# Kernel optimization log

Hardware: AMD Instinct MI355X
Metric: run time of the kernel (lower is better)

Reference implementation:

```python
import jax, jax.numpy as jnp
import numpy as np

EMBED = 768
HEADS = 12
HEAD_DIM = EMBED // HEADS
SCALE = HEAD_DIM ** -0.5


def setup_inputs() -> dict:
    key = jax.random.key(0)
    k1, k2, k3, k4, k5 = jax.random.split(key, 5)
    x = jax.random.normal(k1, (4, 2048, EMBED), dtype=jnp.float32)
    w_qkv = jax.random.normal(k2, (EMBED, 3 * EMBED), dtype=jnp.float32) * (EMBED ** -0.5)
    b_qkv = jax.random.normal(k3, (3 * EMBED,), dtype=jnp.float32) * 0.02
    w_proj = jax.random.normal(k4, (EMBED, EMBED), dtype=jnp.float32) * (EMBED ** -0.5)
    b_proj = jax.random.normal(k5, (EMBED,), dtype=jnp.float32) * 0.02
    return {"x": x, "w_qkv": w_qkv, "b_qkv": b_qkv, "w_proj": w_proj, "b_proj": b_proj}


def reference(x, w_qkv, b_qkv, w_proj, b_proj):
    B, T, D = x.shape
    qkv = x @ w_qkv + b_qkv                      # [B, T, 3D]
    qkv = qkv.reshape(B, T, 3, HEADS, HEAD_DIM)
    qkv = jnp.transpose(qkv, (2, 0, 3, 1, 4))    # [3, B, H, T, hd]
    q, k, v = qkv[0], qkv[1], qkv[2]
    scores = jnp.einsum('bhqd,bhkd->bhqk', q, k) * SCALE
    attn = jax.nn.softmax(scores, axis=-1)       # dropout p=0.0 -> identity
    out = jnp.einsum('bhqk,bhkd->bhqd', attn, v)
    out = jnp.transpose(out, (0, 2, 1, 3)).reshape(B, T, D)
    return out @ w_proj + b_proj
```

## Files before the change

kernel.cpp:

```cpp
#include <hip/hip_runtime.h>
#include <hip/hip_bf16.h>

#define EMBED 768
#define HEADS 12
#define HD 64
#define BATCH 4
#define SEQ 2048
#define M_TOK (BATCH*SEQ)
#define N_QKV (3*EMBED)
#define SL2E 0.18033688011112042f

typedef short bf8 __attribute__((ext_vector_type(8)));
typedef float f4  __attribute__((ext_vector_type(4)));
typedef unsigned short us8 __attribute__((ext_vector_type(8)));

static __device__ inline unsigned short f2bf(float f) {
    unsigned int x = __float_as_uint(f);
    unsigned int r = (x + 0x7fffu + ((x >> 16) & 1u)) >> 16;
    return (unsigned short)r;
}

static __device__ inline unsigned int pack2bf(float a, float b) {
#if defined(__has_builtin)
#if __has_builtin(__builtin_amdgcn_cvt_pk_bf16_f32)
    auto r = __builtin_amdgcn_cvt_pk_bf16_f32(a, b);
    return __builtin_bit_cast(unsigned int, r);
#else
    unsigned int ua = (__float_as_uint(a) + 0x8000u) >> 16;
    unsigned int ub = (__float_as_uint(b) + 0x8000u) & 0xffff0000u;
    return ua | ub;
#endif
#else
    unsigned int ua = (__float_as_uint(a) + 0x8000u) >> 16;
    unsigned int ub = (__float_as_uint(b) + 0x8000u) & 0xffff0000u;
    return ua | ub;
#endif
}

#define GLD_LDS(gp, lp) __builtin_amdgcn_global_load_lds( \
    (const __attribute__((address_space(1))) void*)(gp),  \
    (__attribute__((address_space(3))) void*)(lp), 16, 0, 0)

__global__ void cvt_f32_bf16(const float* __restrict__ in,
                             unsigned short* __restrict__ out, int n) {
    int i = (blockIdx.x * blockDim.x + threadIdx.x) * 4;
    if (i < n) {
        float4 v = *reinterpret_cast<const float4*>(in + i);
        ushort4 o;
        o.x = f2bf(v.x); o.y = f2bf(v.y); o.z = f2bf(v.z); o.w = f2bf(v.w);
        *reinterpret_cast<ushort4*>(out + i) = o;
    }
}

__global__ void transpose_f32_bf16(const float* __restrict__ in,
                                   unsigned short* __restrict__ out, int R, int C,
                                   float scale, int nlim) {
    __shared__ float tile[32][33];
    int c0 = blockIdx.x * 32, r0 = blockIdx.y * 32;
    int tx = threadIdx.x, ty = threadIdx.y;
    for (int i = 0; i < 32; i += 8)
        tile[ty + i][tx] = in[(size_t)(r0 + ty + i) * C + c0 + tx];
    __syncthreads();
    for (int i = 0; i < 32; i += 8) {
        int orow = c0 + ty + i;
        float s = (orow < nlim) ? scale : 1.0f;
        out[(size_t)orow * R + r0 + tx] = f2bf(tile[tx][ty + i] * s);
    }
}

__global__ void scale_bias(const float* __restrict__ in, float* __restrict__ out) {
    int i = blockIdx.x * 256 + threadIdx.x;
    if (i < N_QKV) out[i] = in[i] * (i < 768 ? SL2E : 1.0f);
}

template<int OUT_MODE>
__global__ __launch_bounds__(256) void gemm_bf16(
    const unsigned short* __restrict__ A,
    const unsigned short* __restrict__ BT,
    const float* __restrict__ bias,
    void* __restrict__ Cout, int M, int N, int K)
{
    const int LDA = 32;
    __shared__ unsigned short a_lds[128 * 32];
    __shared__ unsigned short b_lds[128 * 32];
    int tid  = threadIdx.x;
    int lane = tid & 63, w = tid >> 6;
    int quad = lane >> 4, cc = lane & 15;
    int m0 = blockIdx.x * 128, n0 = blockIdx.y * 128;
    int wr = w >> 1, wc = w & 1;
    int mb = wr * 64, nb = wc * 64;
    const unsigned short* Ab = A + (size_t)m0 * K;
    const unsigned short* Bb = BT + (size_t)n0 * K;
    f4 acc[4][4] = {};
    for (int k0 = 0; k0 < K; k0 += 32) {
        __syncthreads();
        for (int p = 0; p < 2; ++p) {
            int li  = p * 256 + tid;
            int row = li >> 2, ch = li & 3;
            GLD_LDS(Ab + (size_t)row * K + k0 + ch * 8, &a_lds[li * 8]);
            GLD_LDS(Bb + (size_t)row * K + k0 + ch * 8, &b_lds[li * 8]);
        }
        __syncthreads();
        bf8 af[4], bfv[4];
        for (int mi = 0; mi < 4; ++mi)
            af[mi] = *reinterpret_cast<const bf8*>(&a_lds[(mb + mi * 16 + cc) * LDA + quad * 8]);
        for (int ni = 0; ni < 4; ++ni)
            bfv[ni] = *reinterpret_cast<const bf8*>(&b_lds[(nb + ni * 16 + cc) * LDA + quad * 8]);
        for (int mi = 0; mi < 4; ++mi)
            for (int ni = 0; ni < 4; ++ni)
                acc[mi][ni] = __builtin_amdgcn_mfma_f32_16x16x32_bf16(af[mi], bfv[ni], acc[mi][ni], 0, 0, 0);
    }
    for (int mi = 0; mi < 4; ++mi)
        for (int ni = 0; ni < 4; ++ni) {
            int gn = n0 + nb + ni * 16 + cc;
            float bv = bias[gn];
            for (int r = 0; r < 4; ++r) {
                int gm = m0 + mb + mi * 16 + quad * 4 + r;
                float v = acc[mi][ni][r] + bv;
                if (OUT_MODE == 0)
                    ((unsigned short*)Cout)[(size_t)gm * N + gn] = f2bf(v);
                else
                    ((float*)Cout)[(size_t)gm * N + gn] = v;
            }
        }
}

__global__ __launch_bounds__(256) void vtrans(
    const unsigned short* __restrict__ qkv, unsigned short* __restrict__ vt)
{
    __shared__ unsigned short lds[64 * 72];
    int tid = threadIdx.x;
    int t0 = blockIdx.x * 64, h = blockIdx.y, b = blockIdx.z;
    for (int p = 0; p < 2; ++p) {
        int li = p * 256 + tid, row = li >> 3, col = li & 7;
        *reinterpret_cast<uint4*>(&lds[row * 72 + col * 8]) =
            *reinterpret_cast<const uint4*>(
                qkv + (size_t)(b * SEQ + t0 + row) * 2304 + 1536 + h * 64 + col * 8);
    }
    __syncthreads();
    for (int p = 0; p < 2; ++p) {
        int li = p * 256 + tid, d = li >> 3, tc = li & 7;
        us8 v;
        for (int j = 0; j < 8; ++j) v[j] = lds[(tc * 8 + j) * 72 + d];
        *reinterpret_cast<us8*>(
            vt + ((size_t)(b * HEADS + h) * 64 + d) * SEQ + t0 + tc * 8) = v;
    }
}

__global__ __launch_bounds__(256, 4) void attn_kernel(
    const unsigned short* __restrict__ qkv,
    const unsigned short* __restrict__ vt,
    unsigned short* __restrict__ out)
{
    const int LDK = 72;
    __shared__ unsigned short k_lds[64 * 72];
    __shared__ unsigned short v_lds[64 * 72];
    __shared__ unsigned short p_lds[128 * 72];
    int tid  = threadIdx.x;
    int lane = tid & 63, w = tid >> 6;
    int quad = lane >> 4, cc = lane & 15;
    int id  = blockIdx.x;
    int sub = id >> 3, rem = id & 7;
    int g   = (sub >> 4) * 8 + rem;
    int qt  = sub & 15;
    int b   = g / HEADS, h = g % HEADS;
    int q0  = qt * 128;

    bf8 qf[2][2];
    for (int nf = 0; nf < 2; ++nf) {
        const unsigned short* qp =
            qkv + (size_t)(b * SEQ + q0 + w * 32 + nf * 16 + cc) * 2304 + h * 64;
        qf[nf][0] = *reinterpret_cast<const bf8*>(qp + quad * 8);
        qf[nf][1] = *reinterpret_cast<const bf8*>(qp + 32 + quad * 8);
    }
    f4 acc[2][4] = {};
    float lsum[2] = {0.f, 0.f};
    const unsigned short* kbase = qkv + (size_t)b * SEQ * 2304 + 768 + h * 64;
    const unsigned short* vbase = vt + (size_t)(b * HEADS + h) * 64 * SEQ;

    for (int kt = 0; kt < SEQ; kt += 64) {
        __syncthreads();
        for (int p = 0; p < 2; ++p) {
            int c   = p * 256 + tid;
            int row = c >> 3, col = c & 7;
            *reinterpret_cast<uint4*>(&k_lds[row * LDK + col * 8]) =
                *reinterpret_cast<const uint4*>(kbase + (size_t)(kt + row) * 2304 + col * 8);
            *reinterpret_cast<uint4*>(&v_lds[row * LDK + col * 8]) =
                *reinterpret_cast<const uint4*>(vbase + (size_t)row * SEQ + kt + col * 8);
        }
        __syncthreads();
        for (int mt = 0; mt < 4; ++mt) {
            bf8 a0 = *reinterpret_cast<const bf8*>(&k_lds[(mt * 16 + cc) * LDK + quad * 8]);
            bf8 a1 = *reinterpret_cast<const bf8*>(&k_lds[(mt * 16 + cc) * LDK + 32 + quad * 8]);
            for (int nf = 0; nf < 2; ++nf) {
                f4 z = {};
                z = __builtin_amdgcn_mfma_f32_16x16x32_bf16(a0, qf[nf][0], z, 0, 0, 0);
                z = __builtin_amdgcn_mfma_f32_16x16x32_bf16(a1, qf[nf][1], z, 0, 0, 0);
                float p0 = exp2f(z[0]), p1 = exp2f(z[1]), p2 = exp2f(z[2]), p3 = exp2f(z[3]);
                lsum[nf] += (p0 + p1) + (p2 + p3);
                uint2 pk;
                pk.x = pack2bf(p0, p1);
                pk.y = pack2bf(p2, p3);
                int ql = w * 32 + nf * 16 + cc;
                *reinterpret_cast<uint2*>(&p_lds[ql * LDK + mt * 16 + quad * 4]) = pk;
            }
        }
        bf8 vb0[4], vb1[4];
        for (int nt = 0; nt < 4; ++nt) {
            vb0[nt] = *reinterpret_cast<const bf8*>(&v_lds[(nt * 16 + cc) * LDK + quad * 8]);
            vb1[nt] = *reinterpret_cast<const bf8*>(&v_lds[(nt * 16 + cc) * LDK + 32 + quad * 8]);
        }
        for (int mf = 0; mf < 2; ++mf) {
            int ql = w * 32 + mf * 16 + cc;
            bf8 a0 = *reinterpret_cast<const bf8*>(&p_lds[ql * LDK + quad * 8]);
            bf8 a1 = *reinterpret_cast<const bf8*>(&p_lds[ql * LDK + 32 + quad * 8]);
            for (int nt = 0; nt < 4; ++nt) {
                acc[mf][nt] = __builtin_amdgcn_mfma_f32_16x16x32_bf16(a0, vb0[nt], acc[mf][nt], 0, 0, 0);
                acc[mf][nt] = __builtin_amdgcn_mfma_f32_16x16x32_bf16(a1, vb1[nt], acc[mf][nt], 0, 0, 0);
            }
        }
    }
    for (int nf = 0; nf < 2; ++nf) {
        lsum[nf] += __shfl_xor(lsum[nf], 16);
        lsum[nf] += __shfl_xor(lsum[nf], 32);
    }
    for (int mf = 0; mf < 2; ++mf)
        for (int r = 0; r < 4; ++r) {
            float L = __shfl(lsum[mf], quad * 4 + r);
            float inv = 1.0f / L;
            int q = q0 + w * 32 + mf * 16 + quad * 4 + r;
            size_t ob = (size_t)(b * SEQ + q) * 768 + h * 64;
            for (int nt = 0; nt < 4; ++nt)
                out[ob + nt * 16 + cc] = f2bf(acc[mf][nt][r] * inv);
        }
}

extern "C" void kernel_launch(void* const* d_in, const int* in_sizes, int n_in,
                              void* d_out, int out_size, void* d_ws, size_t ws_size,
                              hipStream_t stream) {
    const float* x      = (const float*)d_in[0];
    const float* w_qkv  = (const float*)d_in[1];
    const float* b_qkv  = (const float*)d_in[2];
    const float* w_proj = (const float*)d_in[3];
    const float* b_proj = (const float*)d_in[4];
    float* out = (float*)d_out;
    char* ws = (char*)d_ws;
    unsigned short* qkv    = (unsigned short*)(ws);
    unsigned short* vt_buf = (unsigned short*)(ws + 37748736);
    unsigned short* aout   = (unsigned short*)(ws + 50331648);
    unsigned short* xbf    = aout;
    unsigned short* wqkvT  = (unsigned short*)(ws + 62914560);
    unsigned short* wprojT = (unsigned short*)(ws + 66453504);
    float*          bqkv_s = (float*)(ws + 67633152);

    cvt_f32_bf16<<<(M_TOK * EMBED) / 1024, 256, 0, stream>>>(x, xbf, M_TOK * EMBED);
    transpose_f32_bf16<<<dim3(N_QKV / 32, EMBED / 32), dim3(32, 8), 0, stream>>>(
        w_qkv, wqkvT, EMBED, N_QKV, SL2E, 768);
    transpose_f32_bf16<<<dim3(EMBED / 32, EMBED / 32), dim3(32, 8), 0, stream>>>(
        w_proj, wprojT, EMBED, EMBED, 1.0f, 0);
    scale_bias<<<9, 256, 0, stream>>>(b_qkv, bqkv_s);
    gemm_bf16<0><<<dim3(M_TOK / 128, N_QKV / 128), 256, 0, stream>>>(
        xbf, wqkvT, bqkv_s, qkv, M_TOK, N_QKV, EMBED);
    vtrans<<<dim3(SEQ / 64, HEADS, BATCH), 256, 0, stream>>>(qkv, vt_buf);
    attn_kernel<<<768, 256, 0, stream>>>(qkv, vt_buf, aout);
    gemm_bf16<1><<<dim3(M_TOK / 128, EMBED / 128), 256, 0, stream>>>(
        aout, wprojT, b_proj, out, M_TOK, EMBED, EMBED);
}
```

Measured before the change: 273.5 us.

## Use 8 waves per attention block and prefetch next K/V tile into registers

The attention block grows from 256 to 512 threads, so each wave owns 16 query rows instead of 32 and the whole 64-row K/V tile is staged with one load per thread. The next tile's K and V are fetched into registers before the current tile's MFMA work, overlapping global latency with compute. More waves per block should help hide latency and cut register use per wave. The cost is that each wave reloads the V fragments from LDS for fewer rows, and barrier overhead per unit of work rises.

Result: faster. 250.8 us (-8.3%).

```diff
diff --git a/kernel.cpp b/kernel.cpp
--- a/kernel.cpp
+++ b/kernel.cpp
@@ -147,7 +147,7 @@
     }
 }
 
-__global__ __launch_bounds__(256, 4) void attn_kernel(
+__global__ __launch_bounds__(512, 6) void attn_kernel(
     const unsigned short* __restrict__ qkv,
     const unsigned short* __restrict__ vt,
     unsigned short* __restrict__ out)
@@ -166,73 +166,70 @@
     int b   = g / HEADS, h = g % HEADS;
     int q0  = qt * 128;
 
-    bf8 qf[2][2];
-    for (int nf = 0; nf < 2; ++nf) {
+    bf8 qf[2];
+    {
         const unsigned short* qp =
-            qkv + (size_t)(b * SEQ + q0 + w * 32 + nf * 16 + cc) * 2304 + h * 64;
-        qf[nf][0] = *reinterpret_cast<const bf8*>(qp + quad * 8);
-        qf[nf][1] = *reinterpret_cast<const bf8*>(qp + 32 + quad * 8);
-    }
-    f4 acc[2][4] = {};
-    float lsum[2] = {0.f, 0.f};
+            qkv + (size_t)(b * SEQ + q0 + w * 16 + cc) * 2304 + h * 64;
+        qf[0] = *reinterpret_cast<const bf8*>(qp + quad * 8);
+        qf[1] = *reinterpret_cast<const bf8*>(qp + 32 + quad * 8);
+    }
+    f4 acc[4] = {};
+    float lsum = 0.f;
     const unsigned short* kbase = qkv + (size_t)b * SEQ * 2304 + 768 + h * 64;
     const unsigned short* vbase = vt + (size_t)(b * HEADS + h) * 64 * SEQ;
 
+    int srow = tid >> 3, scol = tid & 7;
+    const unsigned short* kp = kbase + (size_t)srow * 2304 + scol * 8;
+    const unsigned short* vp = vbase + (size_t)srow * SEQ + scol * 8;
+    unsigned short* kl = &k_lds[srow * LDK + scol * 8];
+    unsigned short* vl = &v_lds[srow * LDK + scol * 8];
+
+    uint4 kr = *reinterpret_cast<const uint4*>(kp);
+    uint4 vr = *reinterpret_cast<const uint4*>(vp);
+
     for (int kt = 0; kt < SEQ; kt += 64) {
         __syncthreads();
-        for (int p = 0; p < 2; ++p) {
-            int c   = p * 256 + tid;
-            int row = c >> 3, col = c & 7;
-            *reinterpret_cast<uint4*>(&k_lds[row * LDK + col * 8]) =
-                *reinterpret_cast<const uint4*>(kbase + (size_t)(kt + row) * 2304 + col * 8);
-            *reinterpret_cast<uint4*>(&v_lds[row * LDK + col * 8]) =
-                *reinterpret_cast<const uint4*>(vbase + (size_t)row * SEQ + kt + col * 8);
-        }
-        __syncthreads();
+        *reinterpret_cast<uint4*>(kl) = kr;
+        *reinterpret_cast<uint4*>(vl) = vr;
+        __syncthreads();
+        int ktn = kt + 64;
+        if (ktn < SEQ) {
+            kr = *reinterpret_cast<const uint4*>(kp + (size_t)ktn * 2304);
+            vr = *reinterpret_cast<const uint4*>(vp + ktn);
+        }
         for (int mt = 0; mt < 4; ++mt) {
             bf8 a0 = *reinterpret_cast<const bf8*>(&k_lds[(mt * 16 + cc) * LDK + quad * 8]);
             bf8 a1 = *reinterpret_cast<const bf8*>(&k_lds[(mt * 16 + cc) * LDK + 32 + quad * 8]);
-            for (int nf = 0; nf < 2; ++nf) {
-                f4 z = {};
-                z = __builtin_amdgcn_mfma_f32_16x16x32_bf16(a0, qf[nf][0], z, 0, 0, 0);
-                z = __builtin_amdgcn_mfma_f32_16x16x32_bf16(a1, qf[nf][1], z, 0, 0, 0);
-                float p0 = exp2f(z[0]), p1 = exp2f(z[1]), p2 = exp2f(z[2]), p3 = exp2f(z[3]);
-                lsum[nf] += (p0 + p1) + (p2 + p3);
-                uint2 pk;
-                pk.x = pack2bf(p0, p1);
-                pk.y = pack2bf(p2, p3);
-                int ql = w * 32 + nf * 16 + cc;
-                *reinterpret_cast<uint2*>(&p_lds[ql * LDK + mt * 16 + quad * 4]) = pk;
-            }
-        }
-        bf8 vb0[4], vb1[4];
+            f4 z = {};
+            z = __builtin_amdgcn_mfma_f32_16x16x32_bf16(a0, qf[0], z, 0, 0, 0);
+            z = __builtin_amdgcn_mfma_f32_16x16x32_bf16(a1, qf[1], z, 0, 0, 0);
+            float p0 = exp2f(z[0]), p1 = exp2f(z[1]), p2 = exp2f(z[2]), p3 = exp2f(z[3]);
+            lsum += (p0 + p1) + (p2 + p3);
+            uint2 pk;
+            pk.x = pack2bf(p0, p1);
+            pk.y = pack2bf(p2, p3);
+            int ql = w * 16 + cc;
+            *reinterpret_cast<uint2*>(&p_lds[ql * LDK + mt * 16 + quad * 4]) = pk;
+        }
+        bf8 a0 = *reinterpret_cast<const bf8*>(&p_lds[(w * 16 + cc) * LDK + quad * 8]);
+        bf8 a1 = *reinterpret_cast<const bf8*>(&p_lds[(w * 16 + cc) * LDK + 32 + quad * 8]);
         for (int nt = 0; nt < 4; ++nt) {
-            vb0[nt] = *reinterpret_cast<const bf8*>(&v_lds[(nt * 16 + cc) * LDK + quad * 8]);
-            vb1[nt] = *reinterpret_cast<const bf8*>(&v_lds[(nt * 16 + cc) * LDK + 32 + quad * 8]);
-        }
-        for (int mf = 0; mf < 2; ++mf) {
-            int ql = w * 32 + mf * 16 + cc;
-            bf8 a0 = *reinterpret_cast<const bf8*>(&p_lds[ql * LDK + quad * 8]);
-            bf8 a1 = *reinterpret_cast<const bf8*>(&p_lds[ql * LDK + 32 + quad * 8]);
-            for (int nt = 0; nt < 4; ++nt) {
-                acc[mf][nt] = __builtin_amdgcn_mfma_f32_16x16x32_bf16(a0, vb0[nt], acc[mf][nt], 0, 0, 0);
-                acc[mf][nt] = __builtin_amdgcn_mfma_f32_16x16x32_bf16(a1, vb1[nt], acc[mf][nt], 0, 0, 0);
-            }
-        }
-    }
-    for (int nf = 0; nf < 2; ++nf) {
-        lsum[nf] += __shfl_xor(lsum[nf], 16);
-        lsum[nf] += __shfl_xor(lsum[nf], 32);
-    }
-    for (int mf = 0; mf < 2; ++mf)
-        for (int r = 0; r < 4; ++r) {
-            float L = __shfl(lsum[mf], quad * 4 + r);
-            float inv = 1.0f / L;
-            int q = q0 + w * 32 + mf * 16 + quad * 4 + r;
-            size_t ob = (size_t)(b * SEQ + q) * 768 + h * 64;
-            for (int nt = 0; nt < 4; ++nt)
-                out[ob + nt * 16 + cc] = f2bf(acc[mf][nt][r] * inv);
-        }
+            bf8 vb0 = *reinterpret_cast<const bf8*>(&v_lds[(nt * 16 + cc) * LDK + quad * 8]);
+            bf8 vb1 = *reinterpret_cast<const bf8*>(&v_lds[(nt * 16 + cc) * LDK + 32 + quad * 8]);
+            acc[nt] = __builtin_amdgcn_mfma_f32_16x16x32_bf16(a0, vb0, acc[nt], 0, 0, 0);
+            acc[nt] = __builtin_amdgcn_mfma_f32_16x16x32_bf16(a1, vb1, acc[nt], 0, 0, 0);
+        }
+    }
+    lsum += __shfl_xor(lsum, 16);
+    lsum += __shfl_xor(lsum, 32);
+    for (int r = 0; r < 4; ++r) {
+        float L = __shfl(lsum, quad * 4 + r);
+        float inv = 1.0f / L;
+        int q = q0 + w * 16 + quad * 4 + r;
+        size_t ob = (size_t)(b * SEQ + q) * 768 + h * 64;
+        for (int nt = 0; nt < 4; ++nt)
+            out[ob + nt * 16 + cc] = f2bf(acc[nt][r] * inv);
+    }
 }
 
 extern "C" void kernel_launch(void* const* d_in, const int* in_sizes, int n_in,
@@ -262,7 +259,7 @@
     gemm_bf16<0><<<dim3(M_TOK / 128, N_QKV / 128), 256, 0, stream>>>(
         xbf, wqkvT, bqkv_s, qkv, M_TOK, N_QKV, EMBED);
     vtrans<<<dim3(SEQ / 64, HEADS, BATCH), 256, 0, stream>>>(qkv, vt_buf);
-    attn_kernel<<<768, 256, 0, stream>>>(qkv, vt_buf, aout);
+    attn_kernel<<<768, 512, 0, stream>>>(qkv, vt_buf, aout);
     gemm_bf16<1><<<dim3(M_TOK / 128, EMBED / 128), 256, 0, stream>>>(
         aout, wprojT, b_proj, out, M_TOK, EMBED, EMBED);
 }
```
